# Kernel optimization log

Measured on AMD Instinct MI355X. Metric: run time of the kernel, lower is better.

The kernel has to match this reference:

```python
import jax, jax.numpy as jnp
import numpy as np
from jax import lax

N_LAYER = 2
D_MODEL = 256
D_INNER = 512   # expand * d_model
D_STATE = 16
DT_RANK = 16    # ceil(d_model / 16)
D_CONV = 4
VOCAB = 256
B, L = 4, 2048


def setup_inputs() -> dict:
    key = jax.random.key(0)
    ks = jax.random.split(key, 12)
    s = 0.02
    embedding = jax.random.normal(ks[0], (VOCAB, D_MODEL), jnp.float32) * s
    in_proj_w = jax.random.normal(ks[1], (N_LAYER, D_MODEL, 2 * D_INNER), jnp.float32) * s
    conv_w = jax.random.normal(ks[2], (N_LAYER, D_INNER, 1, D_CONV), jnp.float32) * 0.1
    conv_b = jax.random.normal(ks[3], (N_LAYER, D_INNER), jnp.float32) * 0.01
    x_proj_w = jax.random.normal(ks[4], (N_LAYER, D_INNER, DT_RANK + 2 * D_STATE), jnp.float32) * s
    dt_proj_w = jax.random.normal(ks[5], (N_LAYER, DT_RANK, D_INNER), jnp.float32) * (DT_RANK ** -0.5)
    dt_proj_b = jax.random.normal(ks[6], (N_LAYER, D_INNER), jnp.float32) * 0.1
    # S4D-real init: A = -[1..d_state], stored as A_log
    A_log = jnp.log(jnp.broadcast_to(jnp.arange(1, D_STATE + 1, dtype=jnp.float32), (N_LAYER, D_INNER, D_STATE)))
    D = jnp.ones((N_LAYER, D_INNER), jnp.float32)
    out_proj_w = jax.random.normal(ks[7], (N_LAYER, D_INNER, D_MODEL), jnp.float32) * s
    input_ids = jax.random.randint(ks[8], (B, L), 0, VOCAB)
    return {"input_ids": input_ids, "embedding": embedding, "in_proj_w": in_proj_w,
            "conv_w": conv_w, "conv_b": conv_b, "x_proj_w": x_proj_w,
            "dt_proj_w": dt_proj_w, "dt_proj_b": dt_proj_b, "A_log": A_log,
            "D": D, "out_proj_w": out_proj_w}


def _selective_scan(u, delta, A, Bc, Cc):
    # u, delta: [B, L, d_inner]; A: [d_inner, N]; Bc, Cc: [B, L, N]
    def step(h, inp):
        d_t, b_t, c_t, u_t = inp  # [B,d_inner], [B,N], [B,N], [B,d_inner]
        dA = jnp.exp(d_t[:, :, None] * A)                    # [B, d_inner, N]
        h = dA * h + (d_t * u_t)[:, :, None] * b_t[:, None, :]
        y = jnp.sum(h * c_t[:, None, :], axis=-1)            # [B, d_inner]
        return h, y

    h0 = jnp.zeros((u.shape[0], u.shape[2], A.shape[1]), u.dtype)
    xs = (jnp.moveaxis(delta, 1, 0), jnp.moveaxis(Bc, 1, 0),
          jnp.moveaxis(Cc, 1, 0), jnp.moveaxis(u, 1, 0))
    _, ys = lax.scan(step, h0, xs)  # ys: [L, B, d_inner]
    return jnp.moveaxis(ys, 0, 1)


def _mamba_block(x, w_in, w_conv, b_conv, w_xp, w_dt, b_dt, A_log, Dp, w_out):
    # x: [B, L, d_model]
    xz = x @ w_in                                            # [B, L, 2*d_inner]
    u, res = jnp.split(xz, 2, axis=-1)
    # depthwise causal conv1d
    uc = jnp.transpose(u, (0, 2, 1))                          # [B, d_inner, L]
    uc = lax.conv_general_dilated(uc, w_conv, window_strides=(1,),
                                  padding=[(D_CONV - 1, 0)],
                                  feature_group_count=D_INNER,
                                  dimension_numbers=("NCH", "OIH", "NCH"))
    uc = uc + b_conv[None, :, None]
    u = jax.nn.silu(jnp.transpose(uc, (0, 2, 1)))             # [B, L, d_inner]
    x_dbl = u @ w_xp                                          # [B, L, dt_rank + 2N]
    dt, Bc, Cc = jnp.split(x_dbl, [DT_RANK, DT_RANK + D_STATE], axis=-1)
    delta = jax.nn.softplus(dt @ w_dt + b_dt)                 # [B, L, d_inner]
    A = -jnp.exp(A_log)                                       # [d_inner, N]
    y = _selective_scan(u, delta, A, Bc, Cc) + u * Dp
    y = y * jax.nn.silu(res)
    return y @ w_out                                          # [B, L, d_model]


def reference(input_ids, embedding, in_proj_w, conv_w, conv_b, x_proj_w,
              dt_proj_w, dt_proj_b, A_log, D, out_proj_w):
    x = embedding[input_ids]                                  # [B, L, d_model]
    for l in range(N_LAYER):
        x = _mamba_block(x, in_proj_w[l], conv_w[l], conv_b[l], x_proj_w[l],
                         dt_proj_w[l], dt_proj_b[l], A_log[l], D[l], out_proj_w[l])
    return x
```

## Files before the change

### kernel.cpp

```cpp
#include <hip/hip_runtime.h>
#include <math.h>

#define NLAYER 2
#define DMODEL 256
#define DINNER 512
#define DSTATE 16
#define DTRANK 16
#define DCONV  4
#define BB     4
#define LL     2048
#define BL     (BB*LL)
#define NCHUNK 64
#define LC     (LL/NCHUNK)
#define NREC   (BB*DINNER*DSTATE)
#define VOCAB  256

typedef __attribute__((ext_vector_type(8))) short short8;
typedef __attribute__((ext_vector_type(4))) float f32x4;

__device__ __forceinline__ float sigmoidf_(float x) { return 1.0f / (1.0f + __expf(-x)); }

__device__ __forceinline__ unsigned f2bf(float a) {
    unsigned u = __builtin_bit_cast(unsigned, a);
    return (u + 0x7fffu + ((u >> 16) & 1u)) >> 16;
}
__device__ __forceinline__ float bf2f(unsigned h) {
    return __builtin_bit_cast(float, h << 16);
}

__global__ __launch_bounds__(256) void k_cvt_emb(const float* __restrict__ emb,
                                                 ushort* __restrict__ embf) {
    const int v = blockIdx.x;
    const int c = threadIdx.x;
    float s = emb[(size_t)v * DMODEL + c];
    unsigned hi = f2bf(s);
    unsigned lo = f2bf(s - bf2f(hi));
    embf[(size_t)v * (2 * DMODEL) + c] = (ushort)hi;
    embf[(size_t)v * (2 * DMODEL) + DMODEL + c] = (ushort)lo;
}

template<int K>
__global__ __launch_bounds__(256) void k_cvt_w(const float* __restrict__ W,
                                               ushort* __restrict__ F, int N) {
    constexpr int NKF = K / 32;
    const int t = blockIdx.x * 256 + threadIdx.x;
    const int l = t & 63;
    const int cid = t >> 6;
    const int kf = cid % NKF;
    const int nf = cid / NKF;
    const int col = nf * 16 + (l & 15);
    const int k0 = kf * 32 + (l >> 4) * 8;
    float s[8];
#pragma unroll
    for (int j = 0; j < 8; ++j) s[j] = W[(size_t)(k0 + j) * N + col];
    unsigned hi[8], lo[8];
#pragma unroll
    for (int j = 0; j < 8; ++j) {
        hi[j] = f2bf(s[j]);
        lo[j] = f2bf(s[j] - bf2f(hi[j]));
    }
    uint4 ph = make_uint4(hi[0] | (hi[1] << 16), hi[2] | (hi[3] << 16),
                          hi[4] | (hi[5] << 16), hi[6] | (hi[7] << 16));
    uint4 pl = make_uint4(lo[0] | (lo[1] << 16), lo[2] | (lo[3] << 16),
                          lo[4] | (lo[5] << 16), lo[6] | (lo[7] << 16));
    size_t ohi = ((size_t)nf * (2 * NKF) + kf) * 512 + l * 8;
    *(uint4*)&F[ohi] = ph;
    *(uint4*)&F[ohi + (size_t)NKF * 512] = pl;
}

template<int SPLITK, bool IDS>
__global__ __launch_bounds__(256) void k_mgemm(const ushort* __restrict__ A,
                                               const ushort* __restrict__ Bf,
                                               float* __restrict__ C,
                                               int M, int N, int KE,
                                               const int* __restrict__ ids) {
    __shared__ __align__(16) ushort As[8 * 512];
    __shared__ __align__(16) ushort Bs[8 * 512];
    const int tid = threadIdx.x;
    const int w = tid >> 6, lane = tid & 63;
    const int n0 = blockIdx.x * 128, m0 = blockIdx.y * 128;
    const int nkf = KE >> 5;
    const int KT = nkf / SPLITK;
    const int kt0 = blockIdx.z * KT;
    const int wm = w & 1, wn = w >> 1;
    const int c0 = 2 * w, c1 = c0 + 1;

    f32x4 acc[4][4] = {};

    int row0 = m0 + c0 * 16 + (lane & 15);
    int row1 = m0 + c1 * 16 + (lane & 15);
    if (IDS) { row0 = ids[row0]; row1 = ids[row1]; }
    const ushort* Ap0 = A + (size_t)row0 * KE + (lane >> 4) * 8;
    const ushort* Ap1 = A + (size_t)row1 * KE + (lane >> 4) * 8;
    const ushort* Bb0 = Bf + ((size_t)(n0 / 16 + c0) * nkf) * 512 + lane * 8;
    const ushort* Bb1 = Bf + ((size_t)(n0 / 16 + c1) * nkf) * 512 + lane * 8;
    ushort* As0 = As + c0 * 512 + lane * 8;
    ushort* As1 = As + c1 * 512 + lane * 8;
    ushort* Bs0 = Bs + c0 * 512 + lane * 8;
    ushort* Bs1 = Bs + c1 * 512 + lane * 8;

    for (int kt = kt0; kt < kt0 + KT; ++kt) {
        __builtin_amdgcn_global_load_lds((const __attribute__((address_space(1))) void*)(Ap0 + kt * 32),
                                         (__attribute__((address_space(3))) void*)As0, 16, 0, 0);
        __builtin_amdgcn_global_load_lds((const __attribute__((address_space(1))) void*)(Ap1 + kt * 32),
                                         (__attribute__((address_space(3))) void*)As1, 16, 0, 0);
        __builtin_amdgcn_global_load_lds((const __attribute__((address_space(1))) void*)(Bb0 + (size_t)kt * 512),
                                         (__attribute__((address_space(3))) void*)Bs0, 16, 0, 0);
        __builtin_amdgcn_global_load_lds((const __attribute__((address_space(1))) void*)(Bb1 + (size_t)kt * 512),
                                         (__attribute__((address_space(3))) void*)Bs1, 16, 0, 0);
        __syncthreads();
        short8 av[4], bv[4];
#pragma unroll
        for (int i = 0; i < 4; ++i)
            av[i] = *(const short8*)&As[(wm * 4 + i) * 512 + lane * 8];
#pragma unroll
        for (int i = 0; i < 4; ++i)
            bv[i] = *(const short8*)&Bs[(wn * 4 + i) * 512 + lane * 8];
#pragma unroll
        for (int mi = 0; mi < 4; ++mi)
#pragma unroll
            for (int ni = 0; ni < 4; ++ni)
                acc[mi][ni] = __builtin_amdgcn_mfma_f32_16x16x32_bf16(av[mi], bv[ni],
                                                                      acc[mi][ni], 0, 0, 0);
        __syncthreads();
    }

    float* Cw = C + (size_t)blockIdx.z * ((size_t)M * N);
    const int r0 = (lane >> 4) * 4, cc = lane & 15;
#pragma unroll
    for (int mi = 0; mi < 4; ++mi)
#pragma unroll
        for (int r = 0; r < 4; ++r) {
            const int row = m0 + wm * 64 + mi * 16 + r0 + r;
            float* crow = &Cw[(size_t)row * N + n0 + wn * 64 + cc];
#pragma unroll
            for (int ni = 0; ni < 4; ++ni) crow[ni * 16] = acc[mi][ni][r];
        }
}

template<bool TOBF>
__global__ __launch_bounds__(256) void k_red4(const float* __restrict__ p,
                                              float* __restrict__ o,
                                              ushort* __restrict__ xb, int n4) {
    int i = blockIdx.x * 256 + threadIdx.x;
    const float4* p4 = (const float4*)p;
    float4 a = p4[i], b = p4[i + n4], c = p4[i + 2 * n4], d = p4[i + 3 * n4];
    float4 r = make_float4(a.x + b.x + c.x + d.x, a.y + b.y + c.y + d.y,
                           a.z + b.z + c.z + d.z, a.w + b.w + c.w + d.w);
    if (TOBF) {
        const int e0 = i * 4;
        const int bl = e0 >> 8;
        const int cl = e0 & 255;
        float s[4] = {r.x, r.y, r.z, r.w};
        unsigned hi[4], lo[4];
#pragma unroll
        for (int j = 0; j < 4; ++j) {
            hi[j] = f2bf(s[j]);
            lo[j] = f2bf(s[j] - bf2f(hi[j]));
        }
        *(uint2*)&xb[(size_t)bl * 512 + cl] =
            make_uint2(hi[0] | (hi[1] << 16), hi[2] | (hi[3] << 16));
        *(uint2*)&xb[(size_t)bl * 512 + 256 + cl] =
            make_uint2(lo[0] | (lo[1] << 16), lo[2] | (lo[3] << 16));
    } else {
        ((float4*)o)[i] = r;
    }
}

__global__ __launch_bounds__(256) void k_xpd(const float* __restrict__ xz,
                                             const float* __restrict__ cw,
                                             const float* __restrict__ cb,
                                             const float* __restrict__ w_xp,
                                             const float* __restrict__ w_dt,
                                             const float* __restrict__ b_dt,
                                             float* __restrict__ u,
                                             float* __restrict__ Bm,
                                             float* __restrict__ Cm,
                                             float* __restrict__ delta) {
    const int tid = threadIdx.x;
    const int bl0 = blockIdx.x * 16;
    __shared__ float us[16 * DINNER];
    __shared__ float wsx[128 * 48];
    __shared__ float dts[16][DTRANK];

    {
        const int ch0 = tid, ch1 = 256 + tid;
        float4 cwA = *(const float4*)&cw[ch0 * 4];
        float4 cwB = *(const float4*)&cw[ch1 * 4];
        const float cbA = cb[ch0], cbB = cb[ch1];
        const int lbase = bl0 & (LL - 1);
#pragma unroll
        for (int m = 0; m < 16; ++m) {
            const int bl = bl0 + m;
            const int lpos = lbase + m;
            float aA = cbA, aB = cbB;
#pragma unroll
            for (int k = 0; k < DCONV; ++k) {
                int tt = lpos - (DCONV - 1) + k;
                if (tt >= 0) {
                    const float* xr = &xz[(size_t)(bl - (DCONV - 1) + k) * 2 * DINNER];
                    aA = fmaf(((const float*)&cwA)[k], xr[ch0], aA);
                    aB = fmaf(((const float*)&cwB)[k], xr[ch1], aB);
                }
            }
            float uA = aA * sigmoidf_(aA);
            float uB = aB * sigmoidf_(aB);
            us[m * DINNER + ch0] = uA;
            us[m * DINNER + ch1] = uB;
            u[(size_t)bl * DINNER + ch0] = uA;
            u[(size_t)bl * DINNER + ch1] = uB;
        }
    }

    const int mp = tid >> 5;
    const int jg = (tid >> 3) & 3;
    const int s  = tid & 7;
    const float* usm0 = &us[(mp * 2 + 0) * DINNER];
    const float* usm1 = &us[(mp * 2 + 1) * DINNER];

    float acc0[12] = {}, acc1[12] = {};
#pragma unroll 1
    for (int ck = 0; ck < 4; ++ck) {
        __syncthreads();
        {
            const float4* wg = (const float4*)&w_xp[ck * 128 * 48];
            float4* wl = (float4*)wsx;
#pragma unroll
            for (int q = 0; q < 6; ++q) wl[tid + q * 256] = wg[tid + q * 256];
        }
        __syncthreads();
#pragma unroll
        for (int i = 0; i < 16; ++i) {
            const int kl = i * 8 + s;
            const float a0 = usm0[ck * 128 + kl];
            const float a1 = usm1[ck * 128 + kl];
            const float* wr = &wsx[kl * 48 + jg * 12];
            float4 w0 = *(const float4*)&wr[0];
            float4 w1 = *(const float4*)&wr[4];
            float4 w2 = *(const float4*)&wr[8];
            acc0[0]  = fmaf(a0, w0.x, acc0[0]);  acc1[0]  = fmaf(a1, w0.x, acc1[0]);
            acc0[1]  = fmaf(a0, w0.y, acc0[1]);  acc1[1]  = fmaf(a1, w0.y, acc1[1]);
            acc0[2]  = fmaf(a0, w0.z, acc0[2]);  acc1[2]  = fmaf(a1, w0.z, acc1[2]);
            acc0[3]  = fmaf(a0, w0.w, acc0[3]);  acc1[3]  = fmaf(a1, w0.w, acc1[3]);
            acc0[4]  = fmaf(a0, w1.x, acc0[4]);  acc1[4]  = fmaf(a1, w1.x, acc1[4]);
            acc0[5]  = fmaf(a0, w1.y, acc0[5]);  acc1[5]  = fmaf(a1, w1.y, acc1[5]);
            acc0[6]  = fmaf(a0, w1.z, acc0[6]);  acc1[6]  = fmaf(a1, w1.z, acc1[6]);
            acc0[7]  = fmaf(a0, w1.w, acc0[7]);  acc1[7]  = fmaf(a1, w1.w, acc1[7]);
            acc0[8]  = fmaf(a0, w2.x, acc0[8]);  acc1[8]  = fmaf(a1, w2.x, acc1[8]);
            acc0[9]  = fmaf(a0, w2.y, acc0[9]);  acc1[9]  = fmaf(a1, w2.y, acc1[9]);
            acc0[10] = fmaf(a0, w2.z, acc0[10]); acc1[10] = fmaf(a1, w2.z, acc1[10]);
            acc0[11] = fmaf(a0, w2.w, acc0[11]); acc1[11] = fmaf(a1, w2.w, acc1[11]);
        }
    }
#pragma unroll
    for (int off = 4; off >= 1; off >>= 1) {
#pragma unroll
        for (int j = 0; j < 12; ++j) {
            acc0[j] += __shfl_xor(acc0[j], off, 8);
            acc1[j] += __shfl_xor(acc1[j], off, 8);
        }
    }
    if (s < 6) {
        const int bl_a = bl0 + mp * 2 + 0;
        const int bl_b = bl0 + mp * 2 + 1;
#pragma unroll
        for (int q = 0; q < 2; ++q) {
            int j = jg * 12 + s * 2 + q;
            float v0 = acc0[s * 2 + q];
            float v1 = acc1[s * 2 + q];
            if (j < 16) {
                dts[mp * 2 + 0][j] = v0;
                dts[mp * 2 + 1][j] = v1;
            } else if (j < 32) {
                Bm[(size_t)bl_a * DSTATE + (j - 16)] = v0;
                Bm[(size_t)bl_b * DSTATE + (j - 16)] = v1;
            } else {
                Cm[(size_t)bl_a * DSTATE + (j - 32)] = v0;
                Cm[(size_t)bl_b * DSTATE + (j - 32)] = v1;
            }
        }
    }
    __syncthreads();

    const int c0 = (tid & 127) * 4;
    const int mb = (tid >> 7) * 8;
    float4 bd = *(const float4*)&b_dt[c0];
    float a0[8], a1[8], a2[8], a3[8];
#pragma unroll
    for (int t = 0; t < 8; ++t) { a0[t] = bd.x; a1[t] = bd.y; a2[t] = bd.z; a3[t] = bd.w; }
#pragma unroll
    for (int r = 0; r < DTRANK; ++r) {
        float4 w4 = *(const float4*)&w_dt[r * DINNER + c0];
#pragma unroll
        for (int t = 0; t < 8; ++t) {
            float f = dts[mb + t][r];
            a0[t] = fmaf(f, w4.x, a0[t]);
            a1[t] = fmaf(f, w4.y, a1[t]);
            a2[t] = fmaf(f, w4.z, a2[t]);
            a3[t] = fmaf(f, w4.w, a3[t]);
        }
    }
#pragma unroll
    for (int t = 0; t < 8; ++t) {
        float4 o;
        o.x = (a0[t] > 20.f) ? a0[t] : log1pf(__expf(a0[t]));
        o.y = (a1[t] > 20.f) ? a1[t] : log1pf(__expf(a1[t]));
        o.z = (a2[t] > 20.f) ? a2[t] : log1pf(__expf(a2[t]));
        o.w = (a3[t] > 20.f) ? a3[t] : log1pf(__expf(a3[t]));
        *(float4*)&delta[(size_t)(bl0 + mb + t) * DINNER + c0] = o;
    }
}

__global__ __launch_bounds__(256) void k_scan_a(const float* __restrict__ delta,
                                                const float* __restrict__ u,
                                                const float* __restrict__ Bm,
                                                const float* __restrict__ A_log,
                                                float* __restrict__ aprod,
                                                float* __restrict__ hend) {
    const int tid = threadIdx.x;
    const int bid = blockIdx.x;
    const int chalf = bid & 1;
    const int k = (bid >> 1) & (NCHUNK - 1);
    const int b = bid >> 7;
    const int c = chalf * 256 + tid;
    const int bl0 = b * LL + k * LC;

    __shared__ float Bs[LC * DSTATE];
    for (int i = tid; i < LC * DSTATE; i += 256) Bs[i] = Bm[(size_t)bl0 * DSTATE + i];
    __syncthreads();

    float Ac[DSTATE];
#pragma unroll
    for (int q = 0; q < 4; ++q) {
        float4 a = *(const float4*)&A_log[c * DSTATE + q * 4];
        Ac[q * 4 + 0] = -__expf(a.x); Ac[q * 4 + 1] = -__expf(a.y);
        Ac[q * 4 + 2] = -__expf(a.z); Ac[q * 4 + 3] = -__expf(a.w);
    }

    float h[DSTATE] = {};
    float ap[DSTATE];
#pragma unroll
    for (int n = 0; n < DSTATE; ++n) ap[n] = 1.f;

    float dlt = delta[(size_t)bl0 * DINNER + c];
    float uu  = u[(size_t)bl0 * DINNER + c];
    for (int t = 0; t < LC; ++t) {
        float dlt2 = 0.f, uu2 = 0.f;
        if (t + 1 < LC) {
            dlt2 = delta[(size_t)(bl0 + t + 1) * DINNER + c];
            uu2  = u[(size_t)(bl0 + t + 1) * DINNER + c];
        }
        const float w = dlt * uu;
        const float4* Bs4 = (const float4*)&Bs[t * DSTATE];
        float4 b0 = Bs4[0], b1 = Bs4[1], b2 = Bs4[2], b3 = Bs4[3];
        float bv[DSTATE] = {b0.x, b0.y, b0.z, b0.w, b1.x, b1.y, b1.z, b1.w,
                            b2.x, b2.y, b2.z, b2.w, b3.x, b3.y, b3.z, b3.w};
#pragma unroll
        for (int n = 0; n < DSTATE; ++n) {
            float dA = __expf(dlt * Ac[n]);
            ap[n] *= dA;
            h[n] = fmaf(dA, h[n], w * bv[n]);
        }
        dlt = dlt2; uu = uu2;
    }
    size_t base = ((size_t)(k * BB + b) * DINNER + c) * DSTATE;
#pragma unroll
    for (int q = 0; q < 4; ++q) {
        *(float4*)&aprod[base + q * 4] = make_float4(ap[q*4], ap[q*4+1], ap[q*4+2], ap[q*4+3]);
        *(float4*)&hend[base + q * 4]  = make_float4(h[q*4],  h[q*4+1],  h[q*4+2],  h[q*4+3]);
    }
}

__global__ __launch_bounds__(256) void k_scan_b(const float* __restrict__ aprod,
                                                const float* __restrict__ hend,
                                                float* __restrict__ hstart) {
    int i = blockIdx.x * 256 + threadIdx.x;
    float h = 0.f;
#pragma unroll 4
    for (int k = 0; k < NCHUNK; ++k) {
        size_t idx = (size_t)k * NREC + i;
        float a = aprod[idx];
        float e = hend[idx];
        hstart[idx] = h;
        h = fmaf(a, h, e);
    }
}

__global__ __launch_bounds__(256) void k_scan_c(const float* __restrict__ delta,
                                                const float* __restrict__ u,
                                                const float* __restrict__ xz,
                                                const float* __restrict__ Bm,
                                                const float* __restrict__ Cm,
                                                const float* __restrict__ A_log,
                                                const float* __restrict__ Dp,
                                                const float* __restrict__ hstart,
                                                ushort* __restrict__ yb) {
    const int tid = threadIdx.x;
    const int bid = blockIdx.x;
    const int chalf = bid & 1;
    const int k = (bid >> 1) & (NCHUNK - 1);
    const int b = bid >> 7;
    const int c = chalf * 256 + tid;
    const int bl0 = b * LL + k * LC;

    __shared__ float Bs[LC * DSTATE];
    __shared__ float Cs[LC * DSTATE];
    for (int i = tid; i < LC * DSTATE; i += 256) {
        Bs[i] = Bm[(size_t)bl0 * DSTATE + i];
        Cs[i] = Cm[(size_t)bl0 * DSTATE + i];
    }
    __syncthreads();

    float Ac[DSTATE];
#pragma unroll
    for (int q = 0; q < 4; ++q) {
        float4 a = *(const float4*)&A_log[c * DSTATE + q * 4];
        Ac[q * 4 + 0] = -__expf(a.x); Ac[q * 4 + 1] = -__expf(a.y);
        Ac[q * 4 + 2] = -__expf(a.z); Ac[q * 4 + 3] = -__expf(a.w);
    }
    const float Dc = Dp[c];

    float h[DSTATE];
    size_t hbase = ((size_t)(k * BB + b) * DINNER + c) * DSTATE;
#pragma unroll
    for (int q = 0; q < 4; ++q) {
        float4 hv = *(const float4*)&hstart[hbase + q * 4];
        h[q*4] = hv.x; h[q*4+1] = hv.y; h[q*4+2] = hv.z; h[q*4+3] = hv.w;
    }

    float dlt = delta[(size_t)bl0 * DINNER + c];
    float uu  = u[(size_t)bl0 * DINNER + c];
    float rr  = xz[(size_t)bl0 * 2 * DINNER + DINNER + c];
    for (int t = 0; t < LC; ++t) {
        float dlt2 = 0.f, uu2 = 0.f, rr2 = 0.f;
        if (t + 1 < LC) {
            dlt2 = delta[(size_t)(bl0 + t + 1) * DINNER + c];
            uu2  = u[(size_t)(bl0 + t + 1) * DINNER + c];
            rr2  = xz[(size_t)(bl0 + t + 1) * 2 * DINNER + DINNER + c];
        }
        const float w = dlt * uu;
        const float4* Bs4 = (const float4*)&Bs[t * DSTATE];
        float4 b0 = Bs4[0], b1 = Bs4[1], b2 = Bs4[2], b3 = Bs4[3];
        float bv[DSTATE] = {b0.x, b0.y, b0.z, b0.w, b1.x, b1.y, b1.z, b1.w,
                            b2.x, b2.y, b2.z, b2.w, b3.x, b3.y, b3.z, b3.w};
        const float4* Cs4 = (const float4*)&Cs[t * DSTATE];
        float4 c0 = Cs4[0], c1 = Cs4[1], c2 = Cs4[2], c3 = Cs4[3];
        float cv[DSTATE] = {c0.x, c0.y, c0.z, c0.w, c1.x, c1.y, c1.z, c1.w,
                            c2.x, c2.y, c2.z, c2.w, c3.x, c3.y, c3.z, c3.w};
        float s0 = 0.f, s1 = 0.f, s2 = 0.f, s3 = 0.f;
#pragma unroll
        for (int n = 0; n < DSTATE; n += 4) {
            float dA0 = __expf(dlt * Ac[n+0]);
            float dA1 = __expf(dlt * Ac[n+1]);
            float dA2 = __expf(dlt * Ac[n+2]);
            float dA3 = __expf(dlt * Ac[n+3]);
            h[n+0] = fmaf(dA0, h[n+0], w * bv[n+0]);
            h[n+1] = fmaf(dA1, h[n+1], w * bv[n+1]);
            h[n+2] = fmaf(dA2, h[n+2], w * bv[n+2]);
            h[n+3] = fmaf(dA3, h[n+3], w * bv[n+3]);
            s0 = fmaf(h[n+0], cv[n+0], s0);
            s1 = fmaf(h[n+1], cv[n+1], s1);
            s2 = fmaf(h[n+2], cv[n+2], s2);
            s3 = fmaf(h[n+3], cv[n+3], s3);
        }
        float yv = (s0 + s1) + (s2 + s3) + uu * Dc;
        float yg = yv * (rr * sigmoidf_(rr));
        unsigned hi = f2bf(yg);
        unsigned lo = f2bf(yg - bf2f(hi));
        yb[(size_t)(bl0 + t) * (2 * DINNER) + c] = (ushort)hi;
        yb[(size_t)(bl0 + t) * (2 * DINNER) + DINNER + c] = (ushort)lo;
        dlt = dlt2; uu = uu2; rr = rr2;
    }
}

extern "C" void kernel_launch(void* const* d_in, const int* in_sizes, int n_in,
                              void* d_out, int out_size, void* d_ws, size_t ws_size,
                              hipStream_t stream) {
    const int*   ids   = (const int*)d_in[0];
    const float* emb   = (const float*)d_in[1];
    const float* w_in  = (const float*)d_in[2];
    const float* cw    = (const float*)d_in[3];
    const float* cb    = (const float*)d_in[4];
    const float* w_xp  = (const float*)d_in[5];
    const float* w_dt  = (const float*)d_in[6];
    const float* b_dt  = (const float*)d_in[7];
    const float* A_log = (const float*)d_in[8];
    const float* Dp    = (const float*)d_in[9];
    const float* w_out = (const float*)d_in[10];
    float* out = (float*)d_out;

    float* ws = (float*)d_ws;
    float* x    = ws;
    float* xz   = x  + (size_t)BL * DMODEL;
    float* u    = xz + (size_t)BL * 2 * DINNER;
    float* Bm   = u  + (size_t)BL * DINNER;
    float* Cm   = Bm + (size_t)BL * DSTATE;
    float* dlt  = Cm + (size_t)BL * DSTATE;
    float* y    = dlt + (size_t)BL * DINNER;
    float* hend = y + (size_t)BL * DINNER;
    float* wfif = hend + (size_t)NCHUNK * NREC;
    float* wfof = wfif + 262144;
    float* embff = wfof + 131072;
    float* aprod  = x;
    float* hstart = aprod;
    ushort* xb   = (ushort*)x;
    ushort* yb   = (ushort*)y;
    ushort* wfi  = (ushort*)wfif;
    ushort* wfo  = (ushort*)wfof;
    ushort* embf = (ushort*)embff;

    k_cvt_emb<<<VOCAB, DMODEL, 0, stream>>>(emb, embf);

    for (int l = 0; l < NLAYER; ++l) {
        k_cvt_w<DMODEL><<<128, 256, 0, stream>>>(w_in + (size_t)l * DMODEL * 2 * DINNER,
                                                 wfi, 2 * DINNER);
        if (l == 0)
            k_mgemm<1, true><<<dim3(2 * DINNER / 128, BL / 128, 1), 256, 0, stream>>>(
                embf, wfi, xz, BL, 2 * DINNER, 2 * DMODEL, ids);
        else
            k_mgemm<1, false><<<dim3(2 * DINNER / 128, BL / 128, 1), 256, 0, stream>>>(
                xb, wfi, xz, BL, 2 * DINNER, 2 * DMODEL, ids);

        k_xpd<<<BL / 16, 256, 0, stream>>>(xz, cw + l * DINNER * DCONV, cb + l * DINNER,
                                           w_xp + (size_t)l * DINNER * 48,
                                           w_dt + (size_t)l * DTRANK * DINNER,
                                           b_dt + (size_t)l * DINNER, u, Bm, Cm, dlt);

        const float* Al = A_log + (size_t)l * DINNER * DSTATE;
        k_scan_a<<<BB * NCHUNK * 2, 256, 0, stream>>>(dlt, u, Bm, Al, aprod, hend);
        k_scan_b<<<NREC / 256, 256, 0, stream>>>(aprod, hend, hstart);
        k_scan_c<<<BB * NCHUNK * 2, 256, 0, stream>>>(dlt, u, xz, Bm, Cm, Al,
                                                      Dp + (size_t)l * DINNER, hstart, yb);

        k_cvt_w<DINNER><<<64, 256, 0, stream>>>(w_out + (size_t)l * DINNER * DMODEL,
                                                wfo, DMODEL);
        k_mgemm<4, false><<<dim3(DMODEL / 128, BL / 128, 4), 256, 0, stream>>>(
            yb, wfo, xz, BL, DMODEL, 2 * DINNER, ids);
        if (l == NLAYER - 1)
            k_red4<false><<<(BL * DMODEL / 4) / 256, 256, 0, stream>>>(xz, out, xb,
                                                                       BL * DMODEL / 4);
        else
            k_red4<true><<<(BL * DMODEL / 4) / 256, 256, 0, stream>>>(xz, out, xb,
                                                                      BL * DMODEL / 4);
    }
}
```

Baseline: 288.5 us.

## Halve k_xpd row tile, widen K-split to 16 lanes, pad weight smem

The k_xpd kernel now handles 8 rows per block instead of 16, which doubles the grid and halves shared memory for the u tile. The x_proj GEMM remaps threads so 16 lanes split the K dimension instead of 8, with a 16-wide shuffle reduction, and each lane writes one output. The staged weight tile is padded to a stride of 52 floats to reduce LDS bank conflicts. The aim is more blocks and occupancy for this kernel, at the cost of reloading the x_proj weights twice as often across blocks and an extra shuffle stage.

```diff
diff --git a/kernel.cpp b/kernel.cpp
--- a/kernel.cpp
+++ b/kernel.cpp
@@ -14,6 +14,8 @@
 #define LC     (LL/NCHUNK)
 #define NREC   (BB*DINNER*DSTATE)
 #define VOCAB  256
+#define XT     8
+#define WSTR   52
 
 typedef __attribute__((ext_vector_type(8))) short short8;
 typedef __attribute__((ext_vector_type(4))) float f32x4;
@@ -178,10 +180,10 @@
                                              float* __restrict__ Cm,
                                              float* __restrict__ delta) {
     const int tid = threadIdx.x;
-    const int bl0 = blockIdx.x * 16;
-    __shared__ float us[16 * DINNER];
-    __shared__ float wsx[128 * 48];
-    __shared__ float dts[16][DTRANK];
+    const int bl0 = blockIdx.x * XT;
+    __shared__ float us[XT * DINNER];
+    __shared__ float wsx[128 * WSTR];
+    __shared__ float dts[XT][DTRANK];
 
     {
         const int ch0 = tid, ch1 = 256 + tid;
@@ -190,7 +192,7 @@
         const float cbA = cb[ch0], cbB = cb[ch1];
         const int lbase = bl0 & (LL - 1);
 #pragma unroll
-        for (int m = 0; m < 16; ++m) {
+        for (int m = 0; m < XT; ++m) {
             const int bl = bl0 + m;
             const int lpos = lbase + m;
             float aA = cbA, aB = cbB;
@@ -212,9 +214,9 @@
         }
     }
 
-    const int mp = tid >> 5;
-    const int jg = (tid >> 3) & 3;
-    const int s  = tid & 7;
+    const int mp = tid >> 6;
+    const int jg = (tid >> 4) & 3;
+    const int s  = tid & 15;
     const float* usm0 = &us[(mp * 2 + 0) * DINNER];
     const float* usm1 = &us[(mp * 2 + 1) * DINNER];
 
@@ -223,18 +225,21 @@
     for (int ck = 0; ck < 4; ++ck) {
         __syncthreads();
         {
-            const float4* wg = (const float4*)&w_xp[ck * 128 * 48];
-            float4* wl = (float4*)wsx;
-#pragma unroll
-            for (int q = 0; q < 6; ++q) wl[tid + q * 256] = wg[tid + q * 256];
+#pragma unroll
+            for (int q = 0; q < 6; ++q) {
+                int idx = tid + q * 256;
+                int row = idx / 12, col = idx % 12;
+                *(float4*)&wsx[row * WSTR + col * 4] =
+                    *(const float4*)&w_xp[(ck * 128 + row) * 48 + col * 4];
+            }
         }
         __syncthreads();
 #pragma unroll
-        for (int i = 0; i < 16; ++i) {
-            const int kl = i * 8 + s;
+        for (int i = 0; i < 8; ++i) {
+            const int kl = i * 16 + s;
             const float a0 = usm0[ck * 128 + kl];
             const float a1 = usm1[ck * 128 + kl];
-            const float* wr = &wsx[kl * 48 + jg * 12];
+            const float* wr = &wsx[kl * WSTR + jg * 12];
             float4 w0 = *(const float4*)&wr[0];
             float4 w1 = *(const float4*)&wr[4];
             float4 w2 = *(const float4*)&wr[8];
@@ -253,46 +258,43 @@
         }
     }
 #pragma unroll
-    for (int off = 4; off >= 1; off >>= 1) {
+    for (int off = 8; off >= 1; off >>= 1) {
 #pragma unroll
         for (int j = 0; j < 12; ++j) {
-            acc0[j] += __shfl_xor(acc0[j], off, 8);
-            acc1[j] += __shfl_xor(acc1[j], off, 8);
-        }
-    }
-    if (s < 6) {
+            acc0[j] += __shfl_xor(acc0[j], off, 16);
+            acc1[j] += __shfl_xor(acc1[j], off, 16);
+        }
+    }
+    if (s < 12) {
         const int bl_a = bl0 + mp * 2 + 0;
         const int bl_b = bl0 + mp * 2 + 1;
-#pragma unroll
-        for (int q = 0; q < 2; ++q) {
-            int j = jg * 12 + s * 2 + q;
-            float v0 = acc0[s * 2 + q];
-            float v1 = acc1[s * 2 + q];
-            if (j < 16) {
-                dts[mp * 2 + 0][j] = v0;
-                dts[mp * 2 + 1][j] = v1;
-            } else if (j < 32) {
-                Bm[(size_t)bl_a * DSTATE + (j - 16)] = v0;
-                Bm[(size_t)bl_b * DSTATE + (j - 16)] = v1;
-            } else {
-                Cm[(size_t)bl_a * DSTATE + (j - 32)] = v0;
-                Cm[(size_t)bl_b * DSTATE + (j - 32)] = v1;
-            }
+        const int j = jg * 12 + s;
+        const float v0 = acc0[s];
+        const float v1 = acc1[s];
+        if (j < 16) {
+            dts[mp * 2 + 0][j] = v0;
+            dts[mp * 2 + 1][j] = v1;
+        } else if (j < 32) {
+            Bm[(size_t)bl_a * DSTATE + (j - 16)] = v0;
+            Bm[(size_t)bl_b * DSTATE + (j - 16)] = v1;
+        } else {
+            Cm[(size_t)bl_a * DSTATE + (j - 32)] = v0;
+            Cm[(size_t)bl_b * DSTATE + (j - 32)] = v1;
         }
     }
     __syncthreads();
 
     const int c0 = (tid & 127) * 4;
-    const int mb = (tid >> 7) * 8;
+    const int mb = (tid >> 7) * 4;
     float4 bd = *(const float4*)&b_dt[c0];
-    float a0[8], a1[8], a2[8], a3[8];
-#pragma unroll
-    for (int t = 0; t < 8; ++t) { a0[t] = bd.x; a1[t] = bd.y; a2[t] = bd.z; a3[t] = bd.w; }
+    float a0[4], a1[4], a2[4], a3[4];
+#pragma unroll
+    for (int t = 0; t < 4; ++t) { a0[t] = bd.x; a1[t] = bd.y; a2[t] = bd.z; a3[t] = bd.w; }
 #pragma unroll
     for (int r = 0; r < DTRANK; ++r) {
         float4 w4 = *(const float4*)&w_dt[r * DINNER + c0];
 #pragma unroll
-        for (int t = 0; t < 8; ++t) {
+        for (int t = 0; t < 4; ++t) {
             float f = dts[mb + t][r];
             a0[t] = fmaf(f, w4.x, a0[t]);
             a1[t] = fmaf(f, w4.y, a1[t]);
@@ -301,7 +303,7 @@
         }
     }
 #pragma unroll
-    for (int t = 0; t < 8; ++t) {
+    for (int t = 0; t < 4; ++t) {
         float4 o;
         o.x = (a0[t] > 20.f) ? a0[t] : log1pf(__expf(a0[t]));
         o.y = (a1[t] > 20.f) ? a1[t] : log1pf(__expf(a1[t]));
@@ -521,7 +523,7 @@
             k_mgemm<1, false><<<dim3(2 * DINNER / 128, BL / 128, 1), 256, 0, stream>>>(
                 xb, wfi, xz, BL, 2 * DINNER, 2 * DMODEL, ids);
 
-        k_xpd<<<BL / 16, 256, 0, stream>>>(xz, cw + l * DINNER * DCONV, cb + l * DINNER,
+        k_xpd<<<BL / XT, 256, 0, stream>>>(xz, cw + l * DINNER * DCONV, cb + l * DINNER,
                                            w_xp + (size_t)l * DINNER * 48,
                                            w_dt + (size_t)l * DTRANK * DINNER,
                                            b_dt + (size_t)l * DINNER, u, Bm, Cm, dlt);
```

New measurement: 292.7 us. No clear change (+1.4%).

## Split fused conv/x_proj/dt kernel and run x_proj on split-bf16 MFMA GEMM

Applied to the files above, without the earlier changes.

The fused k_xpd kernel is replaced by three stages. A per-element conv+SiLU kernel also writes a hi/lo bf16 copy of u. x_proj then runs through the existing split-K MFMA GEMM with weights zero-padded to 128 columns, followed by a reduction into a padded xdbl buffer. A separate kernel computes delta from xdbl, and the scan kernels now read B and C with a strided layout. This moves the scalar FP32 x_proj work onto matrix cores, at the cost of extra launches, padding waste (48 of 128 columns used) and more intermediate memory traffic.

```diff
diff --git a/kernel.cpp b/kernel.cpp
--- a/kernel.cpp
+++ b/kernel.cpp
@@ -14,6 +14,7 @@
 #define LC     (LL/NCHUNK)
 #define NREC   (BB*DINNER*DSTATE)
 #define VOCAB  256
+#define XDP    128
 
 typedef __attribute__((ext_vector_type(8))) short short8;
 typedef __attribute__((ext_vector_type(4))) float f32x4;
@@ -53,6 +54,36 @@
     float s[8];
 #pragma unroll
     for (int j = 0; j < 8; ++j) s[j] = W[(size_t)(k0 + j) * N + col];
+    unsigned hi[8], lo[8];
+#pragma unroll
+    for (int j = 0; j < 8; ++j) {
+        hi[j] = f2bf(s[j]);
+        lo[j] = f2bf(s[j] - bf2f(hi[j]));
+    }
+    uint4 ph = make_uint4(hi[0] | (hi[1] << 16), hi[2] | (hi[3] << 16),
+                          hi[4] | (hi[5] << 16), hi[6] | (hi[7] << 16));
+    uint4 pl = make_uint4(lo[0] | (lo[1] << 16), lo[2] | (lo[3] << 16),
+                          lo[4] | (lo[5] << 16), lo[6] | (lo[7] << 16));
+    size_t ohi = ((size_t)nf * (2 * NKF) + kf) * 512 + l * 8;
+    *(uint4*)&F[ohi] = ph;
+    *(uint4*)&F[ohi + (size_t)NKF * 512] = pl;
+}
+
+template<int K>
+__global__ __launch_bounds__(256) void k_cvt_wxp(const float* __restrict__ W,
+                                                 ushort* __restrict__ F) {
+    constexpr int NKF = K / 32;
+    const int t = blockIdx.x * 256 + threadIdx.x;
+    const int l = t & 63;
+    const int cid = t >> 6;
+    const int kf = cid % NKF;
+    const int nf = cid / NKF;
+    const int col = nf * 16 + (l & 15);
+    const int k0 = kf * 32 + (l >> 4) * 8;
+    float s[8];
+#pragma unroll
+    for (int j = 0; j < 8; ++j)
+        s[j] = (col < 48) ? W[(size_t)(k0 + j) * 48 + col] : 0.f;
     unsigned hi[8], lo[8];
 #pragma unroll
     for (int j = 0; j < 8; ++j) {
@@ -167,153 +198,76 @@
     }
 }
 
-__global__ __launch_bounds__(256) void k_xpd(const float* __restrict__ xz,
-                                             const float* __restrict__ cw,
-                                             const float* __restrict__ cb,
-                                             const float* __restrict__ w_xp,
-                                             const float* __restrict__ w_dt,
-                                             const float* __restrict__ b_dt,
-                                             float* __restrict__ u,
-                                             float* __restrict__ Bm,
-                                             float* __restrict__ Cm,
-                                             float* __restrict__ delta) {
+__global__ __launch_bounds__(256) void k_conv(const float* __restrict__ xz,
+                                              const float* __restrict__ cw,
+                                              const float* __restrict__ cb,
+                                              float* __restrict__ u,
+                                              ushort* __restrict__ ub) {
+    const int idx = blockIdx.x * 256 + threadIdx.x;
+    const int bl = idx >> 8;
+    const int c0 = (idx & 255) * 2;
+    const int l  = bl & (LL - 1);
+    float4 cwA = *(const float4*)&cw[c0 * 4];
+    float4 cwB = *(const float4*)&cw[c0 * 4 + 4];
+    float2 cbv = *(const float2*)&cb[c0];
+    float aA = cbv.x, aB = cbv.y;
+#pragma unroll
+    for (int k = 0; k < DCONV; ++k) {
+        int t = l - (DCONV - 1) + k;
+        if (t >= 0) {
+            float2 xv = *(const float2*)&xz[(size_t)(bl - (DCONV - 1) + k) * 2 * DINNER + c0];
+            aA = fmaf(((const float*)&cwA)[k], xv.x, aA);
+            aB = fmaf(((const float*)&cwB)[k], xv.y, aB);
+        }
+    }
+    float uA = aA * sigmoidf_(aA);
+    float uB = aB * sigmoidf_(aB);
+    *(float2*)&u[(size_t)bl * DINNER + c0] = make_float2(uA, uB);
+    unsigned hiA = f2bf(uA), loA = f2bf(uA - bf2f(hiA));
+    unsigned hiB = f2bf(uB), loB = f2bf(uB - bf2f(hiB));
+    *(unsigned*)&ub[(size_t)bl * 1024 + c0] = hiA | (hiB << 16);
+    *(unsigned*)&ub[(size_t)bl * 1024 + DINNER + c0] = loA | (loB << 16);
+}
+
+__global__ __launch_bounds__(256) void k_delta(const float* __restrict__ xdbl,
+                                               const float* __restrict__ w_dt,
+                                               const float* __restrict__ b_dt,
+                                               float* __restrict__ delta) {
     const int tid = threadIdx.x;
-    const int bl0 = blockIdx.x * 16;
-    __shared__ float us[16 * DINNER];
-    __shared__ float wsx[128 * 48];
-    __shared__ float dts[16][DTRANK];
-
+    const int bl0 = blockIdx.x * 8;
+    __shared__ float wdt_s[DTRANK * DINNER];
+    __shared__ float dts[8][DTRANK];
     {
-        const int ch0 = tid, ch1 = 256 + tid;
-        float4 cwA = *(const float4*)&cw[ch0 * 4];
-        float4 cwB = *(const float4*)&cw[ch1 * 4];
-        const float cbA = cb[ch0], cbB = cb[ch1];
-        const int lbase = bl0 & (LL - 1);
-#pragma unroll
-        for (int m = 0; m < 16; ++m) {
-            const int bl = bl0 + m;
-            const int lpos = lbase + m;
-            float aA = cbA, aB = cbB;
-#pragma unroll
-            for (int k = 0; k < DCONV; ++k) {
-                int tt = lpos - (DCONV - 1) + k;
-                if (tt >= 0) {
-                    const float* xr = &xz[(size_t)(bl - (DCONV - 1) + k) * 2 * DINNER];
-                    aA = fmaf(((const float*)&cwA)[k], xr[ch0], aA);
-                    aB = fmaf(((const float*)&cwB)[k], xr[ch1], aB);
-                }
-            }
-            float uA = aA * sigmoidf_(aA);
-            float uB = aB * sigmoidf_(aB);
-            us[m * DINNER + ch0] = uA;
-            us[m * DINNER + ch1] = uB;
-            u[(size_t)bl * DINNER + ch0] = uA;
-            u[(size_t)bl * DINNER + ch1] = uB;
-        }
-    }
-
-    const int mp = tid >> 5;
-    const int jg = (tid >> 3) & 3;
-    const int s  = tid & 7;
-    const float* usm0 = &us[(mp * 2 + 0) * DINNER];
-    const float* usm1 = &us[(mp * 2 + 1) * DINNER];
-
-    float acc0[12] = {}, acc1[12] = {};
-#pragma unroll 1
-    for (int ck = 0; ck < 4; ++ck) {
-        __syncthreads();
-        {
-            const float4* wg = (const float4*)&w_xp[ck * 128 * 48];
-            float4* wl = (float4*)wsx;
-#pragma unroll
-            for (int q = 0; q < 6; ++q) wl[tid + q * 256] = wg[tid + q * 256];
-        }
-        __syncthreads();
-#pragma unroll
-        for (int i = 0; i < 16; ++i) {
-            const int kl = i * 8 + s;
-            const float a0 = usm0[ck * 128 + kl];
-            const float a1 = usm1[ck * 128 + kl];
-            const float* wr = &wsx[kl * 48 + jg * 12];
-            float4 w0 = *(const float4*)&wr[0];
-            float4 w1 = *(const float4*)&wr[4];
-            float4 w2 = *(const float4*)&wr[8];
-            acc0[0]  = fmaf(a0, w0.x, acc0[0]);  acc1[0]  = fmaf(a1, w0.x, acc1[0]);
-            acc0[1]  = fmaf(a0, w0.y, acc0[1]);  acc1[1]  = fmaf(a1, w0.y, acc1[1]);
-            acc0[2]  = fmaf(a0, w0.z, acc0[2]);  acc1[2]  = fmaf(a1, w0.z, acc1[2]);
-            acc0[3]  = fmaf(a0, w0.w, acc0[3]);  acc1[3]  = fmaf(a1, w0.w, acc1[3]);
-            acc0[4]  = fmaf(a0, w1.x, acc0[4]);  acc1[4]  = fmaf(a1, w1.x, acc1[4]);
-            acc0[5]  = fmaf(a0, w1.y, acc0[5]);  acc1[5]  = fmaf(a1, w1.y, acc1[5]);
-            acc0[6]  = fmaf(a0, w1.z, acc0[6]);  acc1[6]  = fmaf(a1, w1.z, acc1[6]);
-            acc0[7]  = fmaf(a0, w1.w, acc0[7]);  acc1[7]  = fmaf(a1, w1.w, acc1[7]);
-            acc0[8]  = fmaf(a0, w2.x, acc0[8]);  acc1[8]  = fmaf(a1, w2.x, acc1[8]);
-            acc0[9]  = fmaf(a0, w2.y, acc0[9]);  acc1[9]  = fmaf(a1, w2.y, acc1[9]);
-            acc0[10] = fmaf(a0, w2.z, acc0[10]); acc1[10] = fmaf(a1, w2.z, acc1[10]);
-            acc0[11] = fmaf(a0, w2.w, acc0[11]); acc1[11] = fmaf(a1, w2.w, acc1[11]);
-        }
-    }
-#pragma unroll
-    for (int off = 4; off >= 1; off >>= 1) {
-#pragma unroll
-        for (int j = 0; j < 12; ++j) {
-            acc0[j] += __shfl_xor(acc0[j], off, 8);
-            acc1[j] += __shfl_xor(acc1[j], off, 8);
-        }
-    }
-    if (s < 6) {
-        const int bl_a = bl0 + mp * 2 + 0;
-        const int bl_b = bl0 + mp * 2 + 1;
-#pragma unroll
-        for (int q = 0; q < 2; ++q) {
-            int j = jg * 12 + s * 2 + q;
-            float v0 = acc0[s * 2 + q];
-            float v1 = acc1[s * 2 + q];
-            if (j < 16) {
-                dts[mp * 2 + 0][j] = v0;
-                dts[mp * 2 + 1][j] = v1;
-            } else if (j < 32) {
-                Bm[(size_t)bl_a * DSTATE + (j - 16)] = v0;
-                Bm[(size_t)bl_b * DSTATE + (j - 16)] = v1;
-            } else {
-                Cm[(size_t)bl_a * DSTATE + (j - 32)] = v0;
-                Cm[(size_t)bl_b * DSTATE + (j - 32)] = v1;
-            }
-        }
-    }
+        const float4* wg = (const float4*)w_dt;
+        float4* wl = (float4*)wdt_s;
+#pragma unroll
+        for (int q = 0; q < 8; ++q) wl[tid + q * 256] = wg[tid + q * 256];
+    }
+    if (tid < 128)
+        dts[tid >> 4][tid & 15] = xdbl[(size_t)(bl0 + (tid >> 4)) * XDP + (tid & 15)];
     __syncthreads();
-
-    const int c0 = (tid & 127) * 4;
-    const int mb = (tid >> 7) * 8;
-    float4 bd = *(const float4*)&b_dt[c0];
-    float a0[8], a1[8], a2[8], a3[8];
-#pragma unroll
-    for (int t = 0; t < 8; ++t) { a0[t] = bd.x; a1[t] = bd.y; a2[t] = bd.z; a3[t] = bd.w; }
+    const int m = tid >> 5;
+    const int j = tid & 31;
+    float acc[16];
+#pragma unroll
+    for (int t = 0; t < 16; ++t) acc[t] = b_dt[j + 32 * t];
 #pragma unroll
     for (int r = 0; r < DTRANK; ++r) {
-        float4 w4 = *(const float4*)&w_dt[r * DINNER + c0];
-#pragma unroll
-        for (int t = 0; t < 8; ++t) {
-            float f = dts[mb + t][r];
-            a0[t] = fmaf(f, w4.x, a0[t]);
-            a1[t] = fmaf(f, w4.y, a1[t]);
-            a2[t] = fmaf(f, w4.z, a2[t]);
-            a3[t] = fmaf(f, w4.w, a3[t]);
-        }
-    }
-#pragma unroll
-    for (int t = 0; t < 8; ++t) {
-        float4 o;
-        o.x = (a0[t] > 20.f) ? a0[t] : log1pf(__expf(a0[t]));
-        o.y = (a1[t] > 20.f) ? a1[t] : log1pf(__expf(a1[t]));
-        o.z = (a2[t] > 20.f) ? a2[t] : log1pf(__expf(a2[t]));
-        o.w = (a3[t] > 20.f) ? a3[t] : log1pf(__expf(a3[t]));
-        *(float4*)&delta[(size_t)(bl0 + mb + t) * DINNER + c0] = o;
+        const float dv = dts[m][r];
+#pragma unroll
+        for (int t = 0; t < 16; ++t)
+            acc[t] = fmaf(dv, wdt_s[r * DINNER + j + 32 * t], acc[t]);
+    }
+#pragma unroll
+    for (int t = 0; t < 16; ++t) {
+        float s = acc[t];
+        delta[(size_t)(bl0 + m) * DINNER + j + 32 * t] = (s > 20.f) ? s : log1pf(__expf(s));
     }
 }
 
 __global__ __launch_bounds__(256) void k_scan_a(const float* __restrict__ delta,
                                                 const float* __restrict__ u,
-                                                const float* __restrict__ Bm,
+                                                const float* __restrict__ xdbl,
                                                 const float* __restrict__ A_log,
                                                 float* __restrict__ aprod,
                                                 float* __restrict__ hend) {
@@ -326,7 +280,8 @@
     const int bl0 = b * LL + k * LC;
 
     __shared__ float Bs[LC * DSTATE];
-    for (int i = tid; i < LC * DSTATE; i += 256) Bs[i] = Bm[(size_t)bl0 * DSTATE + i];
+    for (int i = tid; i < LC * DSTATE; i += 256)
+        Bs[i] = xdbl[(size_t)(bl0 + (i >> 4)) * XDP + 16 + (i & 15)];
     __syncthreads();
 
     float Ac[DSTATE];
@@ -389,8 +344,7 @@
 __global__ __launch_bounds__(256) void k_scan_c(const float* __restrict__ delta,
                                                 const float* __restrict__ u,
                                                 const float* __restrict__ xz,
-                                                const float* __restrict__ Bm,
-                                                const float* __restrict__ Cm,
+                                                const float* __restrict__ xdbl,
                                                 const float* __restrict__ A_log,
                                                 const float* __restrict__ Dp,
                                                 const float* __restrict__ hstart,
@@ -406,8 +360,8 @@
     __shared__ float Bs[LC * DSTATE];
     __shared__ float Cs[LC * DSTATE];
     for (int i = tid; i < LC * DSTATE; i += 256) {
-        Bs[i] = Bm[(size_t)bl0 * DSTATE + i];
-        Cs[i] = Cm[(size_t)bl0 * DSTATE + i];
+        Bs[i] = xdbl[(size_t)(bl0 + (i >> 4)) * XDP + 16 + (i & 15)];
+        Cs[i] = xdbl[(size_t)(bl0 + (i >> 4)) * XDP + 32 + (i & 15)];
     }
     __syncthreads();
 
@@ -493,14 +447,15 @@
     float* x    = ws;
     float* xz   = x  + (size_t)BL * DMODEL;
     float* u    = xz + (size_t)BL * 2 * DINNER;
-    float* Bm   = u  + (size_t)BL * DINNER;
-    float* Cm   = Bm + (size_t)BL * DSTATE;
-    float* dlt  = Cm + (size_t)BL * DSTATE;
+    float* dlt  = u  + (size_t)BL * DINNER;
     float* y    = dlt + (size_t)BL * DINNER;
     float* hend = y + (size_t)BL * DINNER;
     float* wfif = hend + (size_t)NCHUNK * NREC;
     float* wfof = wfif + 262144;
     float* embff = wfof + 131072;
+    float* wxff  = embff + 65536;
+    float* xdbl  = wxff + 65536;
+    float* ubf   = xdbl + (size_t)BL * XDP;
     float* aprod  = x;
     float* hstart = aprod;
     ushort* xb   = (ushort*)x;
@@ -508,6 +463,8 @@
     ushort* wfi  = (ushort*)wfif;
     ushort* wfo  = (ushort*)wfof;
     ushort* embf = (ushort*)embff;
+    ushort* wxf  = (ushort*)wxff;
+    ushort* ub   = (ushort*)ubf;
 
     k_cvt_emb<<<VOCAB, DMODEL, 0, stream>>>(emb, embf);
 
@@ -521,15 +478,21 @@
             k_mgemm<1, false><<<dim3(2 * DINNER / 128, BL / 128, 1), 256, 0, stream>>>(
                 xb, wfi, xz, BL, 2 * DINNER, 2 * DMODEL, ids);
 
-        k_xpd<<<BL / 16, 256, 0, stream>>>(xz, cw + l * DINNER * DCONV, cb + l * DINNER,
-                                           w_xp + (size_t)l * DINNER * 48,
-                                           w_dt + (size_t)l * DTRANK * DINNER,
-                                           b_dt + (size_t)l * DINNER, u, Bm, Cm, dlt);
+        k_conv<<<BL, 256, 0, stream>>>(xz, cw + l * DINNER * DCONV, cb + l * DINNER, u, ub);
+
+        k_cvt_wxp<DINNER><<<32, 256, 0, stream>>>(w_xp + (size_t)l * DINNER * 48, wxf);
+        k_mgemm<4, false><<<dim3(1, BL / 128, 4), 256, 0, stream>>>(
+            ub, wxf, dlt, BL, XDP, 2 * DINNER, ids);
+        k_red4<false><<<(BL * XDP / 4) / 256, 256, 0, stream>>>(dlt, xdbl, nullptr,
+                                                               BL * XDP / 4);
+
+        k_delta<<<BL / 8, 256, 0, stream>>>(xdbl, w_dt + (size_t)l * DTRANK * DINNER,
+                                            b_dt + (size_t)l * DINNER, dlt);
 
         const float* Al = A_log + (size_t)l * DINNER * DSTATE;
-        k_scan_a<<<BB * NCHUNK * 2, 256, 0, stream>>>(dlt, u, Bm, Al, aprod, hend);
+        k_scan_a<<<BB * NCHUNK * 2, 256, 0, stream>>>(dlt, u, xdbl, Al, aprod, hend);
         k_scan_b<<<NREC / 256, 256, 0, stream>>>(aprod, hend, hstart);
-        k_scan_c<<<BB * NCHUNK * 2, 256, 0, stream>>>(dlt, u, xz, Bm, Cm, Al,
+        k_scan_c<<<BB * NCHUNK * 2, 256, 0, stream>>>(dlt, u, xz, xdbl, Al,
                                                       Dp + (size_t)l * DINNER, hstart, yb);
 
         k_cvt_w<DINNER><<<64, 256, 0, stream>>>(w_out + (size_t)l * DINNER * DMODEL,
```

New measurement: 365.0 us. 26.5% more time.

## Merge all weight conversions into one launch and chunk conv into xpd loop

Applied to the files above, without the earlier changes.

Replaces the per-layer weight-conversion launches and the embedding conversion with a single k_cvt_all kernel. It converts both layers' in_proj and out_proj weights and the embedding up front into separate buffers, which removes four kernel launches and their serialization points. k_xpd now computes the depthwise conv and SiLU per 128-channel chunk inside the K loop, so shared memory for u shrinks from 16x512 to 16x128 floats. That may raise occupancy, at the cost of more per-chunk work between barriers.

```diff
diff --git a/kernel.cpp b/kernel.cpp
--- a/kernel.cpp
+++ b/kernel.cpp
@@ -28,22 +28,9 @@
     return __builtin_bit_cast(float, h << 16);
 }
 
-__global__ __launch_bounds__(256) void k_cvt_emb(const float* __restrict__ emb,
-                                                 ushort* __restrict__ embf) {
-    const int v = blockIdx.x;
-    const int c = threadIdx.x;
-    float s = emb[(size_t)v * DMODEL + c];
-    unsigned hi = f2bf(s);
-    unsigned lo = f2bf(s - bf2f(hi));
-    embf[(size_t)v * (2 * DMODEL) + c] = (ushort)hi;
-    embf[(size_t)v * (2 * DMODEL) + DMODEL + c] = (ushort)lo;
-}
-
-template<int K>
-__global__ __launch_bounds__(256) void k_cvt_w(const float* __restrict__ W,
-                                               ushort* __restrict__ F, int N) {
-    constexpr int NKF = K / 32;
-    const int t = blockIdx.x * 256 + threadIdx.x;
+__device__ __forceinline__ void cvt_w_body(const float* __restrict__ W,
+                                           ushort* __restrict__ F,
+                                           int N, int NKF, int t) {
     const int l = t & 63;
     const int cid = t >> 6;
     const int kf = cid % NKF;
@@ -66,6 +53,45 @@
     size_t ohi = ((size_t)nf * (2 * NKF) + kf) * 512 + l * 8;
     *(uint4*)&F[ohi] = ph;
     *(uint4*)&F[ohi + (size_t)NKF * 512] = pl;
+}
+
+__global__ __launch_bounds__(256) void k_cvt_all(const float* __restrict__ emb,
+                                                 const float* __restrict__ w_in,
+                                                 const float* __restrict__ w_out,
+                                                 ushort* __restrict__ embf,
+                                                 ushort* __restrict__ wfi0,
+                                                 ushort* __restrict__ wfi1,
+                                                 ushort* __restrict__ wfo0,
+                                                 ushort* __restrict__ wfo1) {
+    const int bid = blockIdx.x;
+    const int tid = threadIdx.x;
+    if (bid < 128) {
+        cvt_w_body(w_in, wfi0, 2 * DINNER, DMODEL / 32, bid * 256 + tid);
+    } else if (bid < 256) {
+        cvt_w_body(w_in + (size_t)DMODEL * 2 * DINNER, wfi1, 2 * DINNER, DMODEL / 32,
+                   (bid - 128) * 256 + tid);
+    } else if (bid < 320) {
+        cvt_w_body(w_out, wfo0, DMODEL, DINNER / 32, (bid - 256) * 256 + tid);
+    } else if (bid < 384) {
+        cvt_w_body(w_out + (size_t)DINNER * DMODEL, wfo1, DMODEL, DINNER / 32,
+                   (bid - 320) * 256 + tid);
+    } else {
+        const int idx = (bid - 384) * 256 + tid;
+        const int v  = idx >> 6;
+        const int c0 = (idx & 63) * 4;
+        float4 sv = *(const float4*)&emb[(size_t)v * DMODEL + c0];
+        float s[4] = {sv.x, sv.y, sv.z, sv.w};
+        unsigned hi[4], lo[4];
+#pragma unroll
+        for (int j = 0; j < 4; ++j) {
+            hi[j] = f2bf(s[j]);
+            lo[j] = f2bf(s[j] - bf2f(hi[j]));
+        }
+        *(uint2*)&embf[(size_t)v * 512 + c0] =
+            make_uint2(hi[0] | (hi[1] << 16), hi[2] | (hi[3] << 16));
+        *(uint2*)&embf[(size_t)v * 512 + 256 + c0] =
+            make_uint2(lo[0] | (lo[1] << 16), lo[2] | (lo[3] << 16));
+    }
 }
 
 template<int SPLITK, bool IDS>
@@ -179,61 +205,56 @@
                                              float* __restrict__ delta) {
     const int tid = threadIdx.x;
     const int bl0 = blockIdx.x * 16;
-    __shared__ float us[16 * DINNER];
+    __shared__ float us[16 * 128];
     __shared__ float wsx[128 * 48];
     __shared__ float dts[16][DTRANK];
-
-    {
-        const int ch0 = tid, ch1 = 256 + tid;
-        float4 cwA = *(const float4*)&cw[ch0 * 4];
-        float4 cwB = *(const float4*)&cw[ch1 * 4];
-        const float cbA = cb[ch0], cbB = cb[ch1];
-        const int lbase = bl0 & (LL - 1);
-#pragma unroll
-        for (int m = 0; m < 16; ++m) {
-            const int bl = bl0 + m;
-            const int lpos = lbase + m;
-            float aA = cbA, aB = cbB;
-#pragma unroll
-            for (int k = 0; k < DCONV; ++k) {
-                int tt = lpos - (DCONV - 1) + k;
-                if (tt >= 0) {
-                    const float* xr = &xz[(size_t)(bl - (DCONV - 1) + k) * 2 * DINNER];
-                    aA = fmaf(((const float*)&cwA)[k], xr[ch0], aA);
-                    aB = fmaf(((const float*)&cwB)[k], xr[ch1], aB);
-                }
-            }
-            float uA = aA * sigmoidf_(aA);
-            float uB = aB * sigmoidf_(aB);
-            us[m * DINNER + ch0] = uA;
-            us[m * DINNER + ch1] = uB;
-            u[(size_t)bl * DINNER + ch0] = uA;
-            u[(size_t)bl * DINNER + ch1] = uB;
-        }
-    }
 
     const int mp = tid >> 5;
     const int jg = (tid >> 3) & 3;
     const int s  = tid & 7;
-    const float* usm0 = &us[(mp * 2 + 0) * DINNER];
-    const float* usm1 = &us[(mp * 2 + 1) * DINNER];
+    const int chl = tid & 127;
+    const int mh  = (tid >> 7) * 8;
+    const int lbase = bl0 & (LL - 1);
 
     float acc0[12] = {}, acc1[12] = {};
 #pragma unroll 1
     for (int ck = 0; ck < 4; ++ck) {
         __syncthreads();
         {
+            const int ch = ck * 128 + chl;
+            float4 cwv = *(const float4*)&cw[ch * 4];
+            const float cbv = cb[ch];
+#pragma unroll
+            for (int m = 0; m < 8; ++m) {
+                const int bl = bl0 + mh + m;
+                const int lpos = lbase + mh + m;
+                float a = cbv;
+#pragma unroll
+                for (int k = 0; k < DCONV; ++k) {
+                    int tt = lpos - (DCONV - 1) + k;
+                    if (tt >= 0)
+                        a = fmaf(((const float*)&cwv)[k],
+                                 xz[(size_t)(bl - (DCONV - 1) + k) * 2 * DINNER + ch], a);
+                }
+                float uv = a * sigmoidf_(a);
+                us[(mh + m) * 128 + chl] = uv;
+                u[(size_t)bl * DINNER + ch] = uv;
+            }
+        }
+        {
             const float4* wg = (const float4*)&w_xp[ck * 128 * 48];
             float4* wl = (float4*)wsx;
 #pragma unroll
             for (int q = 0; q < 6; ++q) wl[tid + q * 256] = wg[tid + q * 256];
         }
         __syncthreads();
+        const float* usm0 = &us[(mp * 2 + 0) * 128];
+        const float* usm1 = &us[(mp * 2 + 1) * 128];
 #pragma unroll
         for (int i = 0; i < 16; ++i) {
             const int kl = i * 8 + s;
-            const float a0 = usm0[ck * 128 + kl];
-            const float a1 = usm1[ck * 128 + kl];
+            const float a0 = usm0[kl];
+            const float a1 = usm1[kl];
             const float* wr = &wsx[kl * 48 + jg * 12];
             float4 w0 = *(const float4*)&wr[0];
             float4 w1 = *(const float4*)&wr[4];
@@ -498,28 +519,29 @@
     float* dlt  = Cm + (size_t)BL * DSTATE;
     float* y    = dlt + (size_t)BL * DINNER;
     float* hend = y + (size_t)BL * DINNER;
-    float* wfif = hend + (size_t)NCHUNK * NREC;
-    float* wfof = wfif + 262144;
-    float* embff = wfof + 131072;
+    float* wfi0f = hend + (size_t)NCHUNK * NREC;
+    float* wfi1f = wfi0f + 262144;
+    float* wfo0f = wfi1f + 262144;
+    float* wfo1f = wfo0f + 131072;
+    float* embff = wfo1f + 131072;
     float* aprod  = x;
     float* hstart = aprod;
     ushort* xb   = (ushort*)x;
     ushort* yb   = (ushort*)y;
-    ushort* wfi  = (ushort*)wfif;
-    ushort* wfo  = (ushort*)wfof;
+    ushort* wfi[2] = {(ushort*)wfi0f, (ushort*)wfi1f};
+    ushort* wfo[2] = {(ushort*)wfo0f, (ushort*)wfo1f};
     ushort* embf = (ushort*)embff;
 
-    k_cvt_emb<<<VOCAB, DMODEL, 0, stream>>>(emb, embf);
+    k_cvt_all<<<448, 256, 0, stream>>>(emb, w_in, w_out, embf,
+                                       wfi[0], wfi[1], wfo[0], wfo[1]);
 
     for (int l = 0; l < NLAYER; ++l) {
-        k_cvt_w<DMODEL><<<128, 256, 0, stream>>>(w_in + (size_t)l * DMODEL * 2 * DINNER,
-                                                 wfi, 2 * DINNER);
         if (l == 0)
             k_mgemm<1, true><<<dim3(2 * DINNER / 128, BL / 128, 1), 256, 0, stream>>>(
-                embf, wfi, xz, BL, 2 * DINNER, 2 * DMODEL, ids);
+                embf, wfi[0], xz, BL, 2 * DINNER, 2 * DMODEL, ids);
         else
             k_mgemm<1, false><<<dim3(2 * DINNER / 128, BL / 128, 1), 256, 0, stream>>>(
-                xb, wfi, xz, BL, 2 * DINNER, 2 * DMODEL, ids);
+                xb, wfi[1], xz, BL, 2 * DINNER, 2 * DMODEL, ids);
 
         k_xpd<<<BL / 16, 256, 0, stream>>>(xz, cw + l * DINNER * DCONV, cb + l * DINNER,
                                            w_xp + (size_t)l * DINNER * 48,
@@ -532,10 +554,8 @@
         k_scan_c<<<BB * NCHUNK * 2, 256, 0, stream>>>(dlt, u, xz, Bm, Cm, Al,
                                                       Dp + (size_t)l * DINNER, hstart, yb);
 
-        k_cvt_w<DINNER><<<64, 256, 0, stream>>>(w_out + (size_t)l * DINNER * DMODEL,
-                                                wfo, DMODEL);
         k_mgemm<4, false><<<dim3(DMODEL / 128, BL / 128, 4), 256, 0, stream>>>(
-            yb, wfo, xz, BL, DMODEL, 2 * DINNER, ids);
+            yb, wfo[l], xz, BL, DMODEL, 2 * DINNER, ids);
         if (l == NLAYER - 1)
             k_red4<false><<<(BL * DMODEL / 4) / 256, 256, 0, stream>>>(xz, out, xb,
                                                                        BL * DMODEL / 4);
```

Result: no change. 286.0 us (-0.9%).
